# Optimization experiments

Measured on AMD Instinct MI355X. Metric: run time of the kernel, lower is better.

Reference implementation:

```python
import jax, jax.numpy as jnp
import numpy as np

D_MODEL = 768
D_INNER = 1536   # expand=2
D_STATE = 16
D_CONV = 4
DT_RANK = 48     # ceil(768/16)
B, T, N = 2, 4, 196


def _rmsnorm(x, w, eps=1e-5):
    var = jnp.mean(x * x, axis=-1, keepdims=True)
    return x * jax.lax.rsqrt(var + eps) * w


def _causal_dwconv(x, w, b):
    # x: (b, l, di), w: (di, k) depthwise, causal left-pad k-1
    xc = jnp.swapaxes(x, 1, 2)  # (b, di, l)
    out = jax.lax.conv_general_dilated(
        xc, w[:, None, :], window_strides=(1,), padding=[(D_CONV - 1, 0)],
        feature_group_count=D_INNER, dimension_numbers=('NCH', 'OIH', 'NCH'))
    return jnp.swapaxes(out + b[None, :, None], 1, 2)


def _selective_scan(u, dt, A, Bm, Cm, Dp):
    # u, dt: (b,l,di); Bm, Cm: (b,l,n); A: (di,n); Dp: (di,)
    dA = jnp.exp(dt[..., None] * A)                    # (b,l,di,n)
    dBu = (dt * u)[..., None] * Bm[:, :, None, :]      # (b,l,di,n)

    def step(h, inp):
        dA_t, dBu_t, C_t = inp
        h = dA_t * h + dBu_t                           # (b,di,n)
        return h, jnp.einsum('bdn,bn->bd', h, C_t)

    h0 = jnp.zeros((u.shape[0], D_INNER, D_STATE), u.dtype)
    _, ys = jax.lax.scan(step, h0, (jnp.swapaxes(dA, 0, 1),
                                    jnp.swapaxes(dBu, 0, 1),
                                    jnp.swapaxes(Cm, 0, 1)))
    return jnp.swapaxes(ys, 0, 1) + u * Dp


def _mamba(x, in_w, cw, cb, xp_w, dt_w, dt_b, A_log, Dp, out_w):
    xz = jnp.einsum('blc,ec->ble', x, in_w)            # (b,l,2*di)
    xb, z = jnp.split(xz, 2, axis=-1)
    xb = jax.nn.silu(_causal_dwconv(xb, cw, cb))
    x_dbl = jnp.einsum('bld,ed->ble', xb, xp_w)        # (b,l,dt_rank+2n)
    dt, Bm, Cm = jnp.split(x_dbl, [DT_RANK, DT_RANK + D_STATE], axis=-1)
    dt = jax.nn.softplus(jnp.einsum('blr,dr->bld', dt, dt_w) + dt_b)
    y = _selective_scan(xb, dt, -jnp.exp(A_log), Bm, Cm, Dp)
    y = y * jax.nn.silu(z)
    return jnp.einsum('bld,cd->blc', y, out_w)


def _block(x, i, norm_w, in_proj_w, conv_w, conv_b, x_proj_w, dt_proj_w,
           dt_proj_b, A_log, D, mix_out_w):
    # residual Mamba block: x + mixer(norm(x)); zero-initialized ssm/conv state
    return x + _mamba(_rmsnorm(x, norm_w[i]), in_proj_w[i], conv_w[i], conv_b[i],
                      x_proj_w[i], dt_proj_w[i], dt_proj_b[i], A_log[i], D[i],
                      mix_out_w[i])


def _bimamba(x, norm_w, in_proj_w, conv_w, conv_b, x_proj_w, dt_proj_w,
             dt_proj_b, A_log, D, mix_out_w, gate_w, gate_b, proj_w, proj_b):
    b, t, n, c = x.shape
    xs = x.reshape(b, t * n, c)
    params = (norm_w, in_proj_w, conv_w, conv_b, x_proj_w, dt_proj_w,
              dt_proj_b, A_log, D, mix_out_w)
    out_f = _block(xs, 0, *params)
    flip_t = lambda y: y.reshape(b, t, n, c)[:, ::-1].reshape(b, t * n, c)
    out_b = flip_t(_block(flip_t(xs), 1, *params))
    gate = jax.nn.sigmoid(
        jnp.einsum('blc,dc->bld', jnp.concatenate([out_f, out_b], -1), gate_w)
        + gate_b)
    out = gate * out_f + (1.0 - gate) * out_b
    out = jnp.einsum('bld,cd->blc', out, proj_w) + proj_b
    return out.reshape(b, t, n, c)


def setup_inputs() -> dict:
    key = jax.random.key(0)
    ks = jax.random.split(key, 12)
    s = 0.02
    a_log = jnp.broadcast_to(
        jnp.log(jnp.arange(1, D_STATE + 1, dtype=jnp.float32)),
        (2, D_INNER, D_STATE)).copy()
    return {
        'x': jax.random.normal(ks[0], (B, T, N, D_MODEL), jnp.float32),
        'norm_w': jnp.ones((2, D_MODEL), jnp.float32),
        'in_proj_w': jax.random.normal(ks[1], (2, 2 * D_INNER, D_MODEL), jnp.float32) * s,
        'conv_w': jax.random.normal(ks[2], (2, D_INNER, D_CONV), jnp.float32) * 0.2,
        'conv_b': jnp.zeros((2, D_INNER), jnp.float32),
        'x_proj_w': jax.random.normal(ks[3], (2, DT_RANK + 2 * D_STATE, D_INNER), jnp.float32) * s,
        'dt_proj_w': jax.random.normal(ks[4], (2, D_INNER, DT_RANK), jnp.float32) * s,
        'dt_proj_b': jax.random.normal(ks[5], (2, D_INNER), jnp.float32) * 0.5 - 4.0,
        'A_log': a_log,
        'D': jnp.ones((2, D_INNER), jnp.float32),
        'mix_out_w': jax.random.normal(ks[6], (2, D_MODEL, D_INNER), jnp.float32) * s,
        'gate_w': jax.random.normal(ks[7], (D_MODEL, 2 * D_MODEL), jnp.float32) * s,
        'gate_b': jnp.zeros((D_MODEL,), jnp.float32),
        'proj_w': jax.random.normal(ks[8], (D_MODEL, D_MODEL), jnp.float32) * s,
        'proj_b': jnp.zeros((D_MODEL,), jnp.float32),
    }


def reference(x, norm_w, in_proj_w, conv_w, conv_b, x_proj_w, dt_proj_w,
              dt_proj_b, A_log, D, mix_out_w, gate_w, gate_b, proj_w, proj_b):
    return _bimamba(x, norm_w, in_proj_w, conv_w, conv_b, x_proj_w, dt_proj_w,
                    dt_proj_b, A_log, D, mix_out_w, gate_w, gate_b, proj_w,
                    proj_b)
```

## Files before the change

### kernel.cpp

```cpp
#include <hip/hip_runtime.h>
#include <cstdint>
#include <cstddef>

#define BB 2
#define TT 4
#define NN 196
#define LL (TT*NN)
#define BLr (BB*LL)
#define CM 768
#define DI 1536
#define DS 16
#define DTR 48
#define XD 80
#define KSL (DI/4)
#define GCH 16
#define LC (LL/GCH)
#define NST (2*BB*DI*DS)

typedef short s16x8 __attribute__((ext_vector_type(8)));
typedef float f32x4 __attribute__((ext_vector_type(4)));

static __device__ __forceinline__ float sigmoidf_(float x) {
  return 1.f / (1.f + __expf(-x));
}
static __device__ __forceinline__ unsigned short f2bf(float f) {
  unsigned int u = __float_as_uint(f);
  unsigned int r = (u + 0x7fffu + ((u >> 16) & 1u)) >> 16;
  return (unsigned short)r;
}
static __device__ __forceinline__ float bf2f(unsigned short u) {
  return __uint_as_float(((unsigned int)u) << 16);
}
static __device__ __forceinline__ float softplusf_(float v) {
  return (v > 20.f) ? v : __logf(1.f + __expf(v));
}
static __device__ __forceinline__ void gload_lds16(const void* g, void* l) {
  __builtin_amdgcn_global_load_lds(
      (const __attribute__((address_space(1))) void*)g,
      (__attribute__((address_space(3))) void*)l, 16, 0, 0);
}

#define S_INW  4718592
#define S_OUTW 2359296
#define S_GATW 1179648
#define S_PRJW 589824
#define S_XPW  245760
#define S_DTW  196608
#define E0 S_INW
#define E1 (E0 + S_OUTW)
#define E2 (E1 + S_GATW)
#define E3 (E2 + S_PRJW)
#define E4 (E3 + S_XPW)
#define E5 (E4 + S_DTW)
#define NCAST ((E5)/256)

__global__ __launch_bounds__(256) void pre_k(const float* __restrict__ x,
    const float* __restrict__ nw, unsigned short* __restrict__ xn,
    const float* __restrict__ in_w, const float* __restrict__ out_w,
    const float* __restrict__ gate_w, const float* __restrict__ proj_w,
    const float* __restrict__ xp_w, const float* __restrict__ dt_w,
    unsigned short* __restrict__ dst)
{
  int blk = blockIdx.x;
  if (blk < 2*BLr) {
    int l   = blk % LL;
    int b   = (blk / LL) % BB;
    int dir = blk / (BB*LL);
    int lsrc = l;
    if (dir == 1) { int t = l / NN, n = l % NN; lsrc = (TT-1-t)*NN + n; }
    const float* xp = x + ((size_t)b*LL + lsrc)*CM;
    float s = 0.f;
    for (int c = threadIdx.x; c < CM; c += 256) { float v = xp[c]; s += v*v; }
    #pragma unroll
    for (int off = 32; off > 0; off >>= 1) s += __shfl_down(s, off);
    __shared__ float red[4];
    if ((threadIdx.x & 63) == 0) red[threadIdx.x >> 6] = s;
    __syncthreads();
    float tot = red[0] + red[1] + red[2] + red[3];
    float r = rsqrtf(tot * (1.f/CM) + 1e-5f);
    const float* w = nw + dir*CM;
    unsigned short* o = xn + (size_t)blk*CM;
    for (int c = threadIdx.x; c < CM; c += 256) o[c] = f2bf(xp[c] * r * w[c]);
  } else {
    int i = (blk - 2*BLr)*256 + threadIdx.x;
    float v;
    if (i < E0)       v = in_w[i];
    else if (i < E1)  v = out_w[i - E0];
    else if (i < E2)  v = gate_w[i - E1];
    else if (i < E3)  v = proj_w[i - E2];
    else if (i < E4)  v = xp_w[i - E3];
    else {
      int j = i - E4, r = j >> 6, c = j & 63;
      v = (c < 48) ? dt_w[r*48 + c] : 0.f;
    }
    dst[i] = f2bf(v);
  }
}

template <int BM, int BN>
__device__ __forceinline__ void gemm_core(
    const unsigned short* __restrict__ A, int lda,
    const unsigned short* __restrict__ W, int ldw,
    int M, int N, int K, int m0, int n0,
    short* As, short* Ws, f32x4 (*acc)[BN/32])
{
  const int tid = threadIdx.x;
  const int wv = tid >> 6, lane = tid & 63;
  const int wm0 = (wv >> 1)*(BM/2), wn0 = (wv & 1)*(BN/2);
  const int lm = lane & 15, g = lane >> 4;
  const int r8 = lane >> 3, ch = lane & 7;
  const int chs = ch ^ r8;
  constexpr int MT = BM/32, NT = BN/32;
  for (int k0 = 0; k0 < K; k0 += 64) {
    #pragma unroll
    for (int e = 0; e < BM/32; ++e) {
      int rb = e*32 + wv*8;
      int gr = m0 + rb + r8; if (gr >= M) gr = M - 1;
      gload_lds16(A + (size_t)gr*lda + k0 + chs*8, &As[rb*64 + lane*8]);
    }
    #pragma unroll
    for (int e = 0; e < BN/32; ++e) {
      int rb = e*32 + wv*8;
      int gn = n0 + rb + r8; if (gn >= N) gn = N - 1;
      gload_lds16(W + (size_t)gn*ldw + k0 + chs*8, &Ws[rb*64 + lane*8]);
    }
    __syncthreads();
    #pragma unroll
    for (int s = 0; s < 2; ++s) {
      s16x8 af[MT], bf[NT];
      #pragma unroll
      for (int i = 0; i < MT; ++i) {
        int R = wm0 + i*16 + lm;
        af[i] = *(const s16x8*)(&As[R*64 + (((s*4 + g) ^ (R & 7))*8)]);
      }
      #pragma unroll
      for (int j = 0; j < NT; ++j) {
        int Rn = wn0 + j*16 + lm;
        bf[j] = *(const s16x8*)(&Ws[Rn*64 + (((s*4 + g) ^ (Rn & 7))*8)]);
      }
      #pragma unroll
      for (int i = 0; i < MT; ++i)
        #pragma unroll
        for (int j = 0; j < NT; ++j)
          acc[i][j] = __builtin_amdgcn_mfma_f32_16x16x32_bf16(af[i], bf[j], acc[i][j], 0, 0, 0);
    }
    __syncthreads();
  }
}

__global__ __launch_bounds__(256, 2) void gemm_in_k(
    const unsigned short* __restrict__ xn, const unsigned short* __restrict__ w,
    unsigned short* __restrict__ xzout)
{
  __shared__ short As[128*64];
  __shared__ short Ws[128*64];
  const int dir = blockIdx.z;
  const unsigned short* A = xn + (size_t)dir*BLr*CM;
  const unsigned short* W = w  + (size_t)dir*2*DI*CM;
  unsigned short* C = xzout + (size_t)dir*BLr*2*DI;
  const int m0 = blockIdx.y*128, n0 = blockIdx.x*128;
  f32x4 acc[4][4];
  #pragma unroll
  for (int i = 0; i < 4; ++i)
    #pragma unroll
    for (int j = 0; j < 4; ++j) acc[i][j] = (f32x4){0.f,0.f,0.f,0.f};
  gemm_core<128,128>(A, CM, W, CM, BLr, 2*DI, CM, m0, n0, As, Ws, acc);
  const int tid = threadIdx.x, wv = tid >> 6, lane = tid & 63;
  const int wm0 = (wv >> 1)*64, wn0 = (wv & 1)*64;
  const int lm = lane & 15, g = lane >> 4;
  #pragma unroll
  for (int i = 0; i < 4; ++i) {
    int row = m0 + wm0 + i*16 + g*4;
    #pragma unroll
    for (int j = 0; j < 4; ++j) {
      int col = n0 + wn0 + j*16 + lm;
      #pragma unroll
      for (int r = 0; r < 4; ++r)
        if (row + r < BLr) C[(size_t)(row + r)*2*DI + col] = f2bf(acc[i][j][r]);
    }
  }
}

__global__ __launch_bounds__(256, 2) void convxproj_k(
    const unsigned short* __restrict__ xz, const float* __restrict__ cw,
    const float* __restrict__ cb, const unsigned short* __restrict__ xpw,
    unsigned short* __restrict__ ub, float* __restrict__ part)
{
  __shared__ short As[128*64];
  __shared__ short Ws[128*64];
  const int ks = blockIdx.x, mt = blockIdx.y, dir = blockIdx.z;
  const int m0 = mt*128;
  const int tid = threadIdx.x;
  const int wv = tid >> 6, lane = tid & 63;
  const int r8 = lane >> 3, ch = lane & 7;
  const int chs = ch ^ r8;
  const int lm = lane & 15, g = lane >> 4;
  const int wm0 = (wv >> 1)*64, wn0 = (wv & 1)*64;
  const unsigned short* XZ = xz + (size_t)dir*BLr*(2*DI);
  const unsigned short* W  = xpw + (size_t)dir*XD*DI + (size_t)ks*KSL;
  unsigned short* UB = ub + (size_t)dir*BLr*DI;
  f32x4 acc[4][4];
  #pragma unroll
  for (int i = 0; i < 4; ++i)
    #pragma unroll
    for (int j = 0; j < 4; ++j) acc[i][j] = (f32x4){0.f,0.f,0.f,0.f};

  for (int k0 = 0; k0 < KSL; k0 += 64) {
    const int di = ks*KSL + k0 + chs*8;
    #pragma unroll
    for (int e = 0; e < 4; ++e) {
      int rb = e*32 + wv*8;
      int gn = rb + r8; if (gn >= XD) gn = XD - 1;
      gload_lds16(W + (size_t)gn*DI + k0 + chs*8, &Ws[rb*64 + lane*8]);
    }
    f32x4 w4[8]; float cbv[8];
    #pragma unroll
    for (int j = 0; j < 8; ++j) {
      w4[j]  = *(const f32x4*)(cw + ((size_t)dir*DI + di + j)*4);
      cbv[j] = cb[dir*DI + di + j];
    }
    #pragma unroll
    for (int e = 0; e < 4; ++e) {
      int rb = e*32 + wv*8;
      int gr = m0 + rb + r8; if (gr >= BLr) gr = BLr - 1;
      int l = gr % LL;
      s16x8 tap[4];
      #pragma unroll
      for (int k = 0; k < 4; ++k) {
        int lp = l - 3 + k;
        if (lp >= 0) tap[k] = *(const s16x8*)(XZ + (size_t)(gr - 3 + k)*(2*DI) + di);
        else         tap[k] = (s16x8){0,0,0,0,0,0,0,0};
      }
      s16x8 outv;
      #pragma unroll
      for (int j = 0; j < 8; ++j) {
        float a = cbv[j];
        #pragma unroll
        for (int k = 0; k < 4; ++k)
          a = fmaf(w4[j][k], bf2f((unsigned short)tap[k][j]), a);
        float v = a * sigmoidf_(a);
        outv[j] = (short)f2bf(v);
      }
      *(s16x8*)(&As[rb*64 + lane*8]) = outv;
      *(s16x8*)(UB + (size_t)gr*DI + di) = outv;
    }
    __syncthreads();
    #pragma unroll
    for (int s = 0; s < 2; ++s) {
      s16x8 af[4], bfr[4];
      #pragma unroll
      for (int i = 0; i < 4; ++i) {
        int R = wm0 + i*16 + lm;
        af[i] = *(const s16x8*)(&As[R*64 + (((s*4 + g) ^ (R & 7))*8)]);
      }
      #pragma unroll
      for (int j = 0; j < 4; ++j) {
        int Rn = wn0 + j*16 + lm;
        bfr[j] = *(const s16x8*)(&Ws[Rn*64 + (((s*4 + g) ^ (Rn & 7))*8)]);
      }
      #pragma unroll
      for (int i = 0; i < 4; ++i)
        #pragma unroll
        for (int j = 0; j < 4; ++j)
          acc[i][j] = __builtin_amdgcn_mfma_f32_16x16x32_bf16(af[i], bfr[j], acc[i][j], 0, 0, 0);
    }
    __syncthreads();
  }
  float* P = part + ((size_t)(dir*4 + ks)*BLr)*XD;
  #pragma unroll
  for (int i = 0; i < 4; ++i) {
    int row = m0 + wm0 + i*16 + g*4;
    #pragma unroll
    for (int j = 0; j < 4; ++j) {
      int col = wn0 + j*16 + lm;
      if (col >= XD) continue;
      #pragma unroll
      for (int r = 0; r < 4; ++r)
        if (row + r < BLr) P[(size_t)(row + r)*XD + col] = acc[i][j][r];
    }
  }
}

__global__ __launch_bounds__(256, 4) void dtx_k(
    const float* __restrict__ part, const unsigned short* __restrict__ dtw,
    const float* __restrict__ dtb, float* __restrict__ dtv,
    float* __restrict__ xdbl)
{
  __shared__ short As[64*64];
  __shared__ short Ws[128*64];
  const int nt = blockIdx.x, mt = blockIdx.y, dir = blockIdx.z;
  const int m0 = mt*64, n0 = nt*128;
  const int tid = threadIdx.x;
  const int wv = tid >> 6, lane = tid & 63;
  const int r8 = lane >> 3, ch = lane & 7;
  const int chs = ch ^ r8;
  const int lm = lane & 15, g = lane >> 4;
  const int wm0 = (wv >> 1)*32, wn0 = (wv & 1)*64;
  const float* P0 = part + ((size_t)(dir*4))*BLr*XD;
  #pragma unroll
  for (int e = 0; e < 2; ++e) {
    int rb = e*32 + wv*8;
    int gr = m0 + rb + r8; if (gr >= BLr) gr = BLr - 1;
    s16x8 outv;
    if (chs < 6) {
      int c = chs*8;
      f32x4 s0 = {0.f,0.f,0.f,0.f}, s1 = {0.f,0.f,0.f,0.f};
      #pragma unroll
      for (int sl = 0; sl < 4; ++sl) {
        const float* p = P0 + ((size_t)sl*BLr + gr)*XD + c;
        s0 += *(const f32x4*)(p);
        s1 += *(const f32x4*)(p + 4);
      }
      #pragma unroll
      for (int j = 0; j < 4; ++j) { outv[j] = (short)f2bf(s0[j]); outv[4+j] = (short)f2bf(s1[j]); }
    } else {
      outv = (s16x8){0,0,0,0,0,0,0,0};
    }
    *(s16x8*)(&As[rb*64 + lane*8]) = outv;
  }
  #pragma unroll
  for (int e = 0; e < 4; ++e) {
    int rb = e*32 + wv*8;
    int gn = n0 + rb + r8;
    gload_lds16(dtw + (size_t)dir*DI*64 + (size_t)gn*64 + chs*8, &Ws[rb*64 + lane*8]);
  }
  __syncthreads();
  f32x4 acc[2][4];
  #pragma unroll
  for (int i = 0; i < 2; ++i)
    #pragma unroll
    for (int j = 0; j < 4; ++j) acc[i][j] = (f32x4){0.f,0.f,0.f,0.f};
  #pragma unroll
  for (int s = 0; s < 2; ++s) {
    s16x8 af[2], bfr[4];
    #pragma unroll
    for (int i = 0; i < 2; ++i) {
      int R = wm0 + i*16 + lm;
      af[i] = *(const s16x8*)(&As[R*64 + (((s*4 + g) ^ (R & 7))*8)]);
    }
    #pragma unroll
    for (int j = 0; j < 4; ++j) {
      int Rn = wn0 + j*16 + lm;
      bfr[j] = *(const s16x8*)(&Ws[Rn*64 + (((s*4 + g) ^ (Rn & 7))*8)]);
    }
    #pragma unroll
    for (int i = 0; i < 2; ++i)
      #pragma unroll
      for (int j = 0; j < 4; ++j)
        acc[i][j] = __builtin_amdgcn_mfma_f32_16x16x32_bf16(af[i], bfr[j], acc[i][j], 0, 0, 0);
  }
  float* C = dtv + (size_t)dir*BLr*DI;
  const float* bias = dtb + (size_t)dir*DI;
  #pragma unroll
  for (int i = 0; i < 2; ++i) {
    int row = m0 + wm0 + i*16 + g*4;
    #pragma unroll
    for (int j = 0; j < 4; ++j) {
      int col = n0 + wn0 + j*16 + lm;
      float bv = bias[col];
      #pragma unroll
      for (int r = 0; r < 4; ++r) {
        if (row + r >= BLr) continue;
        C[(size_t)(row + r)*DI + col] = softplusf_(acc[i][j][r] + bv);
      }
    }
  }
  if (nt == 0) {
    for (int idx = tid; idx < 64*XD; idx += 256) {
      int row = idx / XD, c = idx % XD;
      int gr = m0 + row;
      if (gr >= BLr) continue;
      float s = 0.f;
      #pragma unroll
      for (int sl = 0; sl < 4; ++sl)
        s += P0[((size_t)sl*BLr + gr)*XD + c];
      xdbl[((size_t)dir*BLr + gr)*XD + c] = s;
    }
  }
}

__global__ __launch_bounds__(256) void scanA_k(const float* __restrict__ dtv,
    const unsigned short* __restrict__ u, const float* __restrict__ xdbl,
    const float* __restrict__ A_log, float* __restrict__ carry,
    float* __restrict__ Pm)
{
  int bx = blockIdx.x;
  int g = bx & (GCH-1);
  int rest = bx / GCH;
  int dchunk = rest % (DI/64);
  int b   = (rest / (DI/64)) % BB;
  int dir = rest / ((DI/64)*BB);
  int tid = threadIdx.x;
  int dl = tid >> 2, q = tid & 3;
  int d = dchunk*64 + dl;
  size_t rb = ((size_t)dir*BB + b) * LL + (size_t)g*LC;
  const float* dtp = dtv + rb*DI + d;
  const unsigned short* up = u + rb*DI + d;
  const float* xB  = xdbl + rb*XD + DTR + 4*q;
  f32x4 al = *(const f32x4*)(A_log + ((size_t)dir*DI + d)*DS + 4*q);
  float Av[4];
  #pragma unroll
  for (int i = 0; i < 4; ++i) Av[i] = -__expf(al[i]);
  float h[4] = {0.f,0.f,0.f,0.f};
  float S = 0.f;
  float ndt[2], nu[2]; f32x4 nB[2];
  #pragma unroll
  for (int e = 0; e < 2; ++e) {
    ndt[e] = dtp[(size_t)e*DI];
    nu[e]  = bf2f(up[(size_t)e*DI]);
    nB[e]  = *(const f32x4*)(xB + (size_t)e*XD);
  }
  #pragma unroll 2
  for (int j = 0; j < LC; ++j) {
    int s = j & 1;
    float cdt = ndt[s], cu = nu[s];
    f32x4 cB = nB[s];
    int lp = j + 2;
    if (lp < LC) {
      ndt[s] = dtp[(size_t)lp*DI];
      nu[s]  = bf2f(up[(size_t)lp*DI]);
      nB[s]  = *(const f32x4*)(xB + (size_t)lp*XD);
    }
    float du = cdt * cu;
    S += cdt;
    #pragma unroll
    for (int i = 0; i < 4; ++i) {
      float dA = __expf(cdt * Av[i]);
      h[i] = fmaf(dA, h[i], du * cB[i]);
    }
  }
  size_t sid = (((size_t)(dir*BB + b)*DI + d)*DS + 4*q);
  f32x4 hc = {h[0], h[1], h[2], h[3]};
  f32x4 pc = {__expf(Av[0]*S), __expf(Av[1]*S), __expf(Av[2]*S), __expf(Av[3]*S)};
  *(f32x4*)(carry + (size_t)g*NST + sid) = hc;
  *(f32x4*)(Pm    + (size_t)g*NST + sid) = pc;
}

__global__ __launch_bounds__(256) void scanB_k(float* __restrict__ carry,
    const float* __restrict__ Pm)
{
  int sid = blockIdx.x*256 + threadIdx.x;
  float h = 0.f;
  #pragma unroll
  for (int g = 0; g < GCH; ++g) {
    float c = carry[(size_t)g*NST + sid];
    float p = Pm[(size_t)g*NST + sid];
    carry[(size_t)g*NST + sid] = h;
    h = fmaf(p, h, c);
  }
}

__global__ __launch_bounds__(256) void scanC_k(const float* __restrict__ dtv,
    const unsigned short* __restrict__ u, const unsigned short* __restrict__ xz,
    const float* __restrict__ xdbl, const float* __restrict__ A_log,
    const float* __restrict__ Dp, const float* __restrict__ h_in,
    unsigned short* __restrict__ y)
{
  int bx = blockIdx.x;
  int g = bx & (GCH-1);
  int rest = bx / GCH;
  int dchunk = rest % (DI/64);
  int b   = (rest / (DI/64)) % BB;
  int dir = rest / ((DI/64)*BB);
  int tid = threadIdx.x;
  int dl = tid >> 2, q = tid & 3;
  int d = dchunk*64 + dl;
  size_t rb = ((size_t)dir*BB + b) * LL + (size_t)g*LC;
  const float* dtp = dtv + rb*DI + d;
  const unsigned short* up = u + rb*DI + d;
  const unsigned short* zp = xz + rb*(2*DI) + DI + d;
  const float* xB  = xdbl + rb*XD + DTR + 4*q;
  const float* xC  = xB + DS;
  unsigned short* yp = y + rb*DI + d;
  f32x4 al = *(const f32x4*)(A_log + ((size_t)dir*DI + d)*DS + 4*q);
  float Av[4];
  #pragma unroll
  for (int i = 0; i < 4; ++i) Av[i] = -__expf(al[i]);
  float Dd = Dp[dir*DI + d];
  size_t sid = (((size_t)(dir*BB + b)*DI + d)*DS + 4*q);
  f32x4 h4 = *(const f32x4*)(h_in + (size_t)g*NST + sid);
  float h[4] = {h4[0], h4[1], h4[2], h4[3]};
  float ndt[2], nu[2], nz[2]; f32x4 nB[2], nC[2];
  #pragma unroll
  for (int e = 0; e < 2; ++e) {
    ndt[e] = dtp[(size_t)e*DI];
    nu[e]  = bf2f(up[(size_t)e*DI]);
    nz[e]  = bf2f(zp[(size_t)e*(2*DI)]);
    nB[e]  = *(const f32x4*)(xB + (size_t)e*XD);
    nC[e]  = *(const f32x4*)(xC + (size_t)e*XD);
  }
  #pragma unroll 2
  for (int j = 0; j < LC; ++j) {
    int s = j & 1;
    float cdt = ndt[s], cu = nu[s], cz = nz[s];
    f32x4 cB = nB[s], cC = nC[s];
    int lp = j + 2;
    if (lp < LC) {
      ndt[s] = dtp[(size_t)lp*DI];
      nu[s]  = bf2f(up[(size_t)lp*DI]);
      nz[s]  = bf2f(zp[(size_t)lp*(2*DI)]);
      nB[s]  = *(const f32x4*)(xB + (size_t)lp*XD);
      nC[s]  = *(const f32x4*)(xC + (size_t)lp*XD);
    }
    float du = cdt * cu;
    float acc = 0.f;
    #pragma unroll
    for (int i = 0; i < 4; ++i) {
      float dA = __expf(cdt * Av[i]);
      h[i] = fmaf(dA, h[i], du * cB[i]);
      acc = fmaf(h[i], cC[i], acc);
    }
    acc += __shfl_xor(acc, 1);
    acc += __shfl_xor(acc, 2);
    if (q == 0) {
      float yv = (acc + cu * Dd) * (cz * sigmoidf_(cz));
      yp[(size_t)j*DI] = f2bf(yv);
    }
  }
}

__global__ __launch_bounds__(256, 4) void gemm_outp_k(
    const unsigned short* __restrict__ yb, const unsigned short* __restrict__ w,
    const float* __restrict__ x, unsigned short* __restrict__ cat)
{
  __shared__ short As[64*64];
  __shared__ short Ws[128*64];
  const int dir = blockIdx.z;
  const unsigned short* A = yb + (size_t)dir*BLr*DI;
  const unsigned short* W = w + (size_t)dir*CM*DI;
  const int m0 = blockIdx.y*64, n0 = blockIdx.x*128;
  f32x4 acc[2][4];
  #pragma unroll
  for (int i = 0; i < 2; ++i)
    #pragma unroll
    for (int j = 0; j < 4; ++j) acc[i][j] = (f32x4){0.f,0.f,0.f,0.f};
  gemm_core<64,128>(A, DI, W, DI, BLr, CM, DI, m0, n0, As, Ws, acc);
  const int tid = threadIdx.x, wv = tid >> 6, lane = tid & 63;
  const int wm0 = (wv >> 1)*32, wn0 = (wv & 1)*64;
  const int lm = lane & 15, g = lane >> 4;
  #pragma unroll
  for (int i = 0; i < 2; ++i) {
    int row = m0 + wm0 + i*16 + g*4;
    #pragma unroll
    for (int j = 0; j < 4; ++j) {
      int col = n0 + wn0 + j*16 + lm;
      #pragma unroll
      for (int r = 0; r < 4; ++r) {
        int rr = row + r;
        if (rr >= BLr) continue;
        int rt = rr;
        if (dir == 1) {
          int l = rr % LL, b = rr / LL;
          int t = l / NN, nn = l % NN;
          rt = b*LL + (TT-1-t)*NN + nn;
        }
        float v = x[(size_t)rt*CM + col] + acc[i][j][r];
        cat[(size_t)rt*(2*CM) + dir*CM + col] = f2bf(v);
      }
    }
  }
}

__global__ __launch_bounds__(256, 4) void gemm_gate_k(
    const unsigned short* __restrict__ cat, const unsigned short* __restrict__ w,
    const float* __restrict__ gb, unsigned short* __restrict__ mixb)
{
  __shared__ short As[64*64];
  __shared__ short Ws[64*64];
  const int m0 = blockIdx.y*64, n0 = blockIdx.x*64;
  f32x4 acc[2][2];
  #pragma unroll
  for (int i = 0; i < 2; ++i)
    #pragma unroll
    for (int j = 0; j < 2; ++j) acc[i][j] = (f32x4){0.f,0.f,0.f,0.f};
  gemm_core<64,64>(cat, 2*CM, w, 2*CM, BLr, CM, 2*CM, m0, n0, As, Ws, acc);
  const int tid = threadIdx.x, wv = tid >> 6, lane = tid & 63;
  const int wm0 = (wv >> 1)*32, wn0 = (wv & 1)*32;
  const int lm = lane & 15, g = lane >> 4;
  #pragma unroll
  for (int i = 0; i < 2; ++i) {
    int row = m0 + wm0 + i*16 + g*4;
    #pragma unroll
    for (int j = 0; j < 2; ++j) {
      int col = n0 + wn0 + j*16 + lm;
      float bv = gb[col];
      #pragma unroll
      for (int r = 0; r < 4; ++r) {
        int rr = row + r;
        if (rr >= BLr) continue;
        float gg = sigmoidf_(acc[i][j][r] + bv);
        float fv = bf2f(cat[(size_t)rr*(2*CM) + col]);
        float bo = bf2f(cat[(size_t)rr*(2*CM) + CM + col]);
        mixb[(size_t)rr*CM + col] = f2bf(gg*fv + (1.f - gg)*bo);
      }
    }
  }
}

__global__ __launch_bounds__(256, 4) void gemm_proj_k(
    const unsigned short* __restrict__ mixb, const unsigned short* __restrict__ w,
    const float* __restrict__ pb, float* __restrict__ out)
{
  __shared__ short As[64*64];
  __shared__ short Ws[64*64];
  const int m0 = blockIdx.y*64, n0 = blockIdx.x*64;
  f32x4 acc[2][2];
  #pragma unroll
  for (int i = 0; i < 2; ++i)
    #pragma unroll
    for (int j = 0; j < 2; ++j) acc[i][j] = (f32x4){0.f,0.f,0.f,0.f};
  gemm_core<64,64>(mixb, CM, w, CM, BLr, CM, CM, m0, n0, As, Ws, acc);
  const int tid = threadIdx.x, wv = tid >> 6, lane = tid & 63;
  const int wm0 = (wv >> 1)*32, wn0 = (wv & 1)*32;
  const int lm = lane & 15, g = lane >> 4;
  #pragma unroll
  for (int i = 0; i < 2; ++i) {
    int row = m0 + wm0 + i*16 + g*4;
    #pragma unroll
    for (int j = 0; j < 2; ++j) {
      int col = n0 + wn0 + j*16 + lm;
      float bv = pb[col];
      #pragma unroll
      for (int r = 0; r < 4; ++r)
        if (row + r < BLr) out[(size_t)(row + r)*CM + col] = acc[i][j][r] + bv;
    }
  }
}

extern "C" void kernel_launch(void* const* d_in, const int* in_sizes, int n_in,
                              void* d_out, int out_size, void* d_ws, size_t ws_size,
                              hipStream_t stream)
{
  (void)in_sizes; (void)n_in; (void)out_size; (void)ws_size;
  const float* x      = (const float*)d_in[0];
  const float* norm_w = (const float*)d_in[1];
  const float* in_w   = (const float*)d_in[2];
  const float* conv_w = (const float*)d_in[3];
  const float* conv_b = (const float*)d_in[4];
  const float* xp_w   = (const float*)d_in[5];
  const float* dt_w   = (const float*)d_in[6];
  const float* dt_b   = (const float*)d_in[7];
  const float* A_log  = (const float*)d_in[8];
  const float* Dp     = (const float*)d_in[9];
  const float* out_w  = (const float*)d_in[10];
  const float* gate_w = (const float*)d_in[11];
  const float* gate_b = (const float*)d_in[12];
  const float* proj_w = (const float*)d_in[13];
  const float* proj_b = (const float*)d_in[14];
  float* out = (float*)d_out;
  char* wsb  = (char*)d_ws;

  unsigned short* w_all   = (unsigned short*)(wsb + 0);
  unsigned short* in_w_b  = w_all;
  unsigned short* out_w_b = w_all + E0;
  unsigned short* gate_w_b= w_all + E1;
  unsigned short* proj_w_b= w_all + E2;
  unsigned short* xp_w_b  = w_all + E3;
  unsigned short* dt_w_b  = w_all + E4;
  unsigned short* xz_b = (unsigned short*)(wsb + 18579456);
  unsigned short* ub   = (unsigned short*)(wsb + 37847040);
  float* xdbl  = (float*)(wsb + 57114624);
  float* dtvb  = (float*)(wsb + 58118144);
  unsigned short* y_b = (unsigned short*)(wsb + 77385728);
  unsigned short* tmp = (unsigned short*)(wsb + 87019520);
  unsigned short* cat_b = (unsigned short*)(wsb + 106287104);
  unsigned short* mix_b = (unsigned short*)(wsb + 111104000);

  unsigned short* xn_b = tmp;
  float* part = (float*)(wsb + 0);
  float* carry = (float*)(wsb + 0);
  float* Pmat  = (float*)(wsb + 87019520 + 524288);

  pre_k<<<2*BLr + NCAST, 256, 0, stream>>>(
      x, norm_w, xn_b, in_w, out_w, gate_w, proj_w, xp_w, dt_w, w_all);
  gemm_in_k<<<dim3(3072/128, (BLr+127)/128, 2), 256, 0, stream>>>(
      xn_b, in_w_b, xz_b);
  convxproj_k<<<dim3(4, (BLr+127)/128, 2), 256, 0, stream>>>(
      xz_b, conv_w, conv_b, xp_w_b, ub, part);
  dtx_k<<<dim3(DI/128, (BLr+63)/64, 2), 256, 0, stream>>>(
      part, dt_w_b, dt_b, dtvb, xdbl);
  scanA_k<<<2*BB*(DI/64)*GCH, 256, 0, stream>>>(
      dtvb, ub, xdbl, A_log, carry, Pmat);
  scanB_k<<<NST/256, 256, 0, stream>>>(carry, Pmat);
  scanC_k<<<2*BB*(DI/64)*GCH, 256, 0, stream>>>(
      dtvb, ub, xz_b, xdbl, A_log, Dp, carry, y_b);
  gemm_outp_k<<<dim3(CM/128, (BLr+63)/64, 2), 256, 0, stream>>>(
      y_b, out_w_b, x, cat_b);
  gemm_gate_k<<<dim3(CM/64, (BLr+63)/64, 1), 256, 0, stream>>>(
      cat_b, gate_w_b, gate_b, mix_b);
  gemm_proj_k<<<dim3(CM/64, (BLr+63)/64, 1), 256, 0, stream>>>(
      mix_b, proj_w_b, proj_b, out);
}
```

Before: 317.7 us.

## Fuse all stages into one persistent megakernel with software grid barriers

```diff
diff --git a/kernel.cpp b/kernel.cpp
--- a/kernel.cpp
+++ b/kernel.cpp
@@ -12,10 +12,10 @@
 #define DS 16
 #define DTR 48
 #define XD 80
-#define KSL (DI/4)
 #define GCH 16
 #define LC (LL/GCH)
 #define NST (2*BB*DI*DS)
+#define NB 512
 
 typedef short s16x8 __attribute__((ext_vector_type(8)));
 typedef float f32x4 __attribute__((ext_vector_type(4)));
@@ -52,53 +52,40 @@
 #define E3 (E2 + S_PRJW)
 #define E4 (E3 + S_XPW)
 #define E5 (E4 + S_DTW)
-#define NCAST ((E5)/256)
-
-__global__ __launch_bounds__(256) void pre_k(const float* __restrict__ x,
-    const float* __restrict__ nw, unsigned short* __restrict__ xn,
-    const float* __restrict__ in_w, const float* __restrict__ out_w,
-    const float* __restrict__ gate_w, const float* __restrict__ proj_w,
-    const float* __restrict__ xp_w, const float* __restrict__ dt_w,
-    unsigned short* __restrict__ dst)
-{
-  int blk = blockIdx.x;
-  if (blk < 2*BLr) {
-    int l   = blk % LL;
-    int b   = (blk / LL) % BB;
-    int dir = blk / (BB*LL);
-    int lsrc = l;
-    if (dir == 1) { int t = l / NN, n = l % NN; lsrc = (TT-1-t)*NN + n; }
-    const float* xp = x + ((size_t)b*LL + lsrc)*CM;
-    float s = 0.f;
-    for (int c = threadIdx.x; c < CM; c += 256) { float v = xp[c]; s += v*v; }
-    #pragma unroll
-    for (int off = 32; off > 0; off >>= 1) s += __shfl_down(s, off);
-    __shared__ float red[4];
-    if ((threadIdx.x & 63) == 0) red[threadIdx.x >> 6] = s;
-    __syncthreads();
-    float tot = red[0] + red[1] + red[2] + red[3];
-    float r = rsqrtf(tot * (1.f/CM) + 1e-5f);
-    const float* w = nw + dir*CM;
-    unsigned short* o = xn + (size_t)blk*CM;
-    for (int c = threadIdx.x; c < CM; c += 256) o[c] = f2bf(xp[c] * r * w[c]);
-  } else {
-    int i = (blk - 2*BLr)*256 + threadIdx.x;
-    float v;
-    if (i < E0)       v = in_w[i];
-    else if (i < E1)  v = out_w[i - E0];
-    else if (i < E2)  v = gate_w[i - E1];
-    else if (i < E3)  v = proj_w[i - E2];
-    else if (i < E4)  v = xp_w[i - E3];
-    else {
-      int j = i - E4, r = j >> 6, c = j & 63;
-      v = (c < 48) ? dt_w[r*48 + c] : 0.f;
-    }
-    dst[i] = f2bf(v);
-  }
+
+#define O_WALL  0u
+#define O_XZ    18579456u
+#define O_UB    37847040u
+#define O_XDBLB 47480832u
+#define O_XDBL  48000000u
+#define O_DTV   50000000u
+#define O_Y     70000000u
+#define O_CARRY 80000000u
+#define O_PM    87000000u
+#define O_XN    94000000u
+#define O_PART  99000000u
+#define O_CAT   112000000u
+#define O_MIX   117000000u
+#define O_OPART 120000000u
+#define O_GPART 149000000u
+#define O_PPART 178000000u
+#define O_BAR   198000000u
+
+static __device__ __forceinline__ void gridbar(int* bar, int slot) {
+  __syncthreads();
+  if (threadIdx.x == 0) {
+    __threadfence();
+    atomicAdd(&bar[slot], 1);
+    while (__hip_atomic_load(&bar[slot], __ATOMIC_RELAXED,
+                             __HIP_MEMORY_SCOPE_AGENT) < NB)
+      __builtin_amdgcn_s_sleep(1);
+    __threadfence();
+  }
+  __syncthreads();
 }
 
 template <int BM, int BN>
-__device__ __forceinline__ void gemm_core(
+static __device__ __forceinline__ void gemm_core(
     const unsigned short* __restrict__ A, int lda,
     const unsigned short* __restrict__ W, int ldw,
     int M, int N, int K, int m0, int n0,
@@ -148,23 +135,9 @@
   }
 }
 
-__global__ __launch_bounds__(256, 2) void gemm_in_k(
-    const unsigned short* __restrict__ xn, const unsigned short* __restrict__ w,
-    unsigned short* __restrict__ xzout)
+static __device__ __forceinline__ void epi_part(
+    f32x4 (*acc)[4], float* P, int ldp, int m0, int n0)
 {
-  __shared__ short As[128*64];
-  __shared__ short Ws[128*64];
-  const int dir = blockIdx.z;
-  const unsigned short* A = xn + (size_t)dir*BLr*CM;
-  const unsigned short* W = w  + (size_t)dir*2*DI*CM;
-  unsigned short* C = xzout + (size_t)dir*BLr*2*DI;
-  const int m0 = blockIdx.y*128, n0 = blockIdx.x*128;
-  f32x4 acc[4][4];
-  #pragma unroll
-  for (int i = 0; i < 4; ++i)
-    #pragma unroll
-    for (int j = 0; j < 4; ++j) acc[i][j] = (f32x4){0.f,0.f,0.f,0.f};
-  gemm_core<128,128>(A, CM, W, CM, BLr, 2*DI, CM, m0, n0, As, Ws, acc);
   const int tid = threadIdx.x, wv = tid >> 6, lane = tid & 63;
   const int wm0 = (wv >> 1)*64, wn0 = (wv & 1)*64;
   const int lm = lane & 15, g = lane >> 4;
@@ -176,454 +149,469 @@
       int col = n0 + wn0 + j*16 + lm;
       #pragma unroll
       for (int r = 0; r < 4; ++r)
-        if (row + r < BLr) C[(size_t)(row + r)*2*DI + col] = f2bf(acc[i][j][r]);
-    }
-  }
-}
-
-__global__ __launch_bounds__(256, 2) void convxproj_k(
-    const unsigned short* __restrict__ xz, const float* __restrict__ cw,
-    const float* __restrict__ cb, const unsigned short* __restrict__ xpw,
-    unsigned short* __restrict__ ub, float* __restrict__ part)
+        if (row + r < BLr) P[(size_t)(row + r)*ldp + col] = acc[i][j][r];
+    }
+  }
+}
+static __device__ __forceinline__ void epi_bf16(
+    f32x4 (*acc)[4], unsigned short* C, int ldc, int m0, int n0)
 {
+  const int tid = threadIdx.x, wv = tid >> 6, lane = tid & 63;
+  const int wm0 = (wv >> 1)*64, wn0 = (wv & 1)*64;
+  const int lm = lane & 15, g = lane >> 4;
+  #pragma unroll
+  for (int i = 0; i < 4; ++i) {
+    int row = m0 + wm0 + i*16 + g*4;
+    #pragma unroll
+    for (int j = 0; j < 4; ++j) {
+      int col = n0 + wn0 + j*16 + lm;
+      #pragma unroll
+      for (int r = 0; r < 4; ++r)
+        if (row + r < BLr) C[(size_t)(row + r)*ldc + col] = f2bf(acc[i][j][r]);
+    }
+  }
+}
+
+__global__ __launch_bounds__(256, 2) void mega_k(
+    const float* __restrict__ x, const float* __restrict__ norm_w,
+    const float* __restrict__ in_w, const float* __restrict__ conv_w,
+    const float* __restrict__ conv_b, const float* __restrict__ xp_w,
+    const float* __restrict__ dt_w, const float* __restrict__ dt_b,
+    const float* __restrict__ A_log, const float* __restrict__ Dp,
+    const float* __restrict__ out_w, const float* __restrict__ gate_w,
+    const float* __restrict__ gate_b, const float* __restrict__ proj_w,
+    const float* __restrict__ proj_b, float* __restrict__ out,
+    char* __restrict__ wsb)
+{
+  unsigned short* w_all  = (unsigned short*)(wsb + O_WALL);
+  unsigned short* out_w_b  = w_all + E0;
+  unsigned short* gate_w_b = w_all + E1;
+  unsigned short* proj_w_b = w_all + E2;
+  unsigned short* xp_w_b   = w_all + E3;
+  unsigned short* dt_w_b   = w_all + E4;
+  unsigned short* xz_b   = (unsigned short*)(wsb + O_XZ);
+  unsigned short* ub     = (unsigned short*)(wsb + O_UB);
+  unsigned short* xdbl_b = (unsigned short*)(wsb + O_XDBLB);
+  float* xdbl   = (float*)(wsb + O_XDBL);
+  float* dtvb   = (float*)(wsb + O_DTV);
+  unsigned short* y_b    = (unsigned short*)(wsb + O_Y);
+  float* carry  = (float*)(wsb + O_CARRY);
+  float* Pmat   = (float*)(wsb + O_PM);
+  unsigned short* xn_b   = (unsigned short*)(wsb + O_XN);
+  float* part   = (float*)(wsb + O_PART);
+  unsigned short* cat_b  = (unsigned short*)(wsb + O_CAT);
+  unsigned short* mix_b  = (unsigned short*)(wsb + O_MIX);
+  float* opart  = (float*)(wsb + O_OPART);
+  float* gpart  = (float*)(wsb + O_GPART);
+  float* ppart  = (float*)(wsb + O_PPART);
+  int* bar      = (int*)(wsb + O_BAR);
+
   __shared__ short As[128*64];
   __shared__ short Ws[128*64];
-  const int ks = blockIdx.x, mt = blockIdx.y, dir = blockIdx.z;
-  const int m0 = mt*128;
-  const int tid = threadIdx.x;
+  __shared__ float red[4];
+
+  const int bid = blockIdx.x, tid = threadIdx.x;
   const int wv = tid >> 6, lane = tid & 63;
   const int r8 = lane >> 3, ch = lane & 7;
   const int chs = ch ^ r8;
-  const int lm = lane & 15, g = lane >> 4;
-  const int wm0 = (wv >> 1)*64, wn0 = (wv & 1)*64;
-  const unsigned short* XZ = xz + (size_t)dir*BLr*(2*DI);
-  const unsigned short* W  = xpw + (size_t)dir*XD*DI + (size_t)ks*KSL;
-  unsigned short* UB = ub + (size_t)dir*BLr*DI;
-  f32x4 acc[4][4];
-  #pragma unroll
-  for (int i = 0; i < 4; ++i)
-    #pragma unroll
-    for (int j = 0; j < 4; ++j) acc[i][j] = (f32x4){0.f,0.f,0.f,0.f};
-
-  for (int k0 = 0; k0 < KSL; k0 += 64) {
-    const int di = ks*KSL + k0 + chs*8;
-    #pragma unroll
-    for (int e = 0; e < 4; ++e) {
-      int rb = e*32 + wv*8;
-      int gn = rb + r8; if (gn >= XD) gn = XD - 1;
-      gload_lds16(W + (size_t)gn*DI + k0 + chs*8, &Ws[rb*64 + lane*8]);
-    }
-    f32x4 w4[8]; float cbv[8];
-    #pragma unroll
-    for (int j = 0; j < 8; ++j) {
-      w4[j]  = *(const f32x4*)(cw + ((size_t)dir*DI + di + j)*4);
-      cbv[j] = cb[dir*DI + di + j];
-    }
-    #pragma unroll
-    for (int e = 0; e < 4; ++e) {
-      int rb = e*32 + wv*8;
-      int gr = m0 + rb + r8; if (gr >= BLr) gr = BLr - 1;
-      int l = gr % LL;
-      s16x8 tap[4];
-      #pragma unroll
-      for (int k = 0; k < 4; ++k) {
-        int lp = l - 3 + k;
-        if (lp >= 0) tap[k] = *(const s16x8*)(XZ + (size_t)(gr - 3 + k)*(2*DI) + di);
-        else         tap[k] = (s16x8){0,0,0,0,0,0,0,0};
-      }
-      s16x8 outv;
+  const int lm = lane & 15, g4 = lane >> 4;
+
+  for (int row = bid; row < 2*BLr; row += NB) {
+    int l   = row % LL;
+    int b   = (row / LL) % BB;
+    int dir = row / (BB*LL);
+    int lsrc = l;
+    if (dir == 1) { int t = l / NN, n = l % NN; lsrc = (TT-1-t)*NN + n; }
+    const float* xp = x + ((size_t)b*LL + lsrc)*CM;
+    float s = 0.f;
+    for (int c = tid; c < CM; c += 256) { float v = xp[c]; s += v*v; }
+    #pragma unroll
+    for (int off = 32; off > 0; off >>= 1) s += __shfl_down(s, off);
+    if ((tid & 63) == 0) red[tid >> 6] = s;
+    __syncthreads();
+    float tot = red[0] + red[1] + red[2] + red[3];
+    float rs = rsqrtf(tot * (1.f/CM) + 1e-5f);
+    const float* w = norm_w + dir*CM;
+    unsigned short* o = xn_b + (size_t)row*CM;
+    for (int c = tid; c < CM; c += 256) o[c] = f2bf(xp[c] * rs * w[c]);
+    __syncthreads();
+  }
+  for (int i = bid*256 + tid; i < E5; i += NB*256) {
+    float v;
+    if (i < E0)       v = in_w[i];
+    else if (i < E1)  v = out_w[i - E0];
+    else if (i < E2)  v = gate_w[i - E1];
+    else if (i < E3)  v = proj_w[i - E2];
+    else if (i < E4)  v = xp_w[i - E3];
+    else {
+      int j = i - E4, r = j >> 6, c = j & 63;
+      v = (c < 48) ? dt_w[r*48 + c] : 0.f;
+    }
+    w_all[i] = f2bf(v);
+  }
+  gridbar(bar, 0);
+
+  for (int t = bid; t < 624; t += NB) {
+    int nt = t % 24, mt = (t/24) % 13, dir = t/312;
+    const unsigned short* A = xn_b + (size_t)dir*BLr*CM;
+    const unsigned short* W = w_all + (size_t)dir*2*DI*CM;
+    unsigned short* C = xz_b + (size_t)dir*BLr*2*DI;
+    f32x4 acc[4][4];
+    #pragma unroll
+    for (int i = 0; i < 4; ++i)
+      #pragma unroll
+      for (int j = 0; j < 4; ++j) acc[i][j] = (f32x4){0.f,0.f,0.f,0.f};
+    gemm_core<128,128>(A, CM, W, CM, BLr, 2*DI, CM, mt*128, nt*128, As, Ws, acc);
+    epi_bf16(acc, C, 2*DI, mt*128, nt*128);
+  }
+  gridbar(bar, 1);
+
+  for (int t = bid; t < 312; t += NB) {
+    int ks = t % 12, mt = (t/12) % 13, dir = t/156;
+    const int m0 = mt*128;
+    const int wm0 = (wv >> 1)*64, wn0 = (wv & 1)*64;
+    const unsigned short* XZ = xz_b + (size_t)dir*BLr*(2*DI);
+    const unsigned short* W  = xp_w_b + (size_t)dir*XD*DI + ks*128;
+    unsigned short* UB = ub + (size_t)dir*BLr*DI;
+    f32x4 acc[4][4];
+    #pragma unroll
+    for (int i = 0; i < 4; ++i)
+      #pragma unroll
+      for (int j = 0; j < 4; ++j) acc[i][j] = (f32x4){0.f,0.f,0.f,0.f};
+    for (int k0 = 0; k0 < 128; k0 += 64) {
+      const int di = ks*128 + k0 + chs*8;
+      #pragma unroll
+      for (int e = 0; e < 4; ++e) {
+        int rb = e*32 + wv*8;
+        int gn = rb + r8; if (gn >= XD) gn = XD - 1;
+        gload_lds16(W + (size_t)gn*DI + k0 + chs*8, &Ws[rb*64 + lane*8]);
+      }
+      f32x4 w4[8]; float cbv[8];
       #pragma unroll
       for (int j = 0; j < 8; ++j) {
-        float a = cbv[j];
-        #pragma unroll
-        for (int k = 0; k < 4; ++k)
-          a = fmaf(w4[j][k], bf2f((unsigned short)tap[k][j]), a);
-        float v = a * sigmoidf_(a);
-        outv[j] = (short)f2bf(v);
-      }
-      *(s16x8*)(&As[rb*64 + lane*8]) = outv;
-      *(s16x8*)(UB + (size_t)gr*DI + di) = outv;
-    }
-    __syncthreads();
-    #pragma unroll
-    for (int s = 0; s < 2; ++s) {
-      s16x8 af[4], bfr[4];
+        w4[j]  = *(const f32x4*)(conv_w + ((size_t)dir*DI + di + j)*4);
+        cbv[j] = conv_b[dir*DI + di + j];
+      }
+      #pragma unroll
+      for (int e = 0; e < 4; ++e) {
+        int rb = e*32 + wv*8;
+        int gr = m0 + rb + r8; if (gr >= BLr) gr = BLr - 1;
+        int l = gr % LL;
+        s16x8 tap[4];
+        #pragma unroll
+        for (int k = 0; k < 4; ++k) {
+          int lp = l - 3 + k;
+          if (lp >= 0) tap[k] = *(const s16x8*)(XZ + (size_t)(gr - 3 + k)*(2*DI) + di);
+          else         tap[k] = (s16x8){0,0,0,0,0,0,0,0};
+        }
+        s16x8 outv;
+        #pragma unroll
+        for (int j = 0; j < 8; ++j) {
+          float a = cbv[j];
+          #pragma unroll
+          for (int k = 0; k < 4; ++k)
+            a = fmaf(w4[j][k], bf2f((unsigned short)tap[k][j]), a);
+          float v = a * sigmoidf_(a);
+          outv[j] = (short)f2bf(v);
+        }
+        *(s16x8*)(&As[rb*64 + lane*8]) = outv;
+        *(s16x8*)(UB + (size_t)gr*DI + di) = outv;
+      }
+      __syncthreads();
+      #pragma unroll
+      for (int s = 0; s < 2; ++s) {
+        s16x8 af[4], bfr[4];
+        #pragma unroll
+        for (int i = 0; i < 4; ++i) {
+          int R = wm0 + i*16 + lm;
+          af[i] = *(const s16x8*)(&As[R*64 + (((s*4 + g4) ^ (R & 7))*8)]);
+        }
+        #pragma unroll
+        for (int j = 0; j < 4; ++j) {
+          int Rn = wn0 + j*16 + lm;
+          bfr[j] = *(const s16x8*)(&Ws[Rn*64 + (((s*4 + g4) ^ (Rn & 7))*8)]);
+        }
+        #pragma unroll
+        for (int i = 0; i < 4; ++i)
+          #pragma unroll
+          for (int j = 0; j < 4; ++j)
+            acc[i][j] = __builtin_amdgcn_mfma_f32_16x16x32_bf16(af[i], bfr[j], acc[i][j], 0, 0, 0);
+      }
+      __syncthreads();
+    }
+    float* P = part + ((size_t)(dir*12 + ks)*BLr)*XD;
+    #pragma unroll
+    for (int i = 0; i < 4; ++i) {
+      int row = m0 + wm0 + i*16 + g4*4;
+      #pragma unroll
+      for (int j = 0; j < 4; ++j) {
+        int col = wn0 + j*16 + lm;
+        if (col >= XD) continue;
+        #pragma unroll
+        for (int r = 0; r < 4; ++r)
+          if (row + r < BLr) P[(size_t)(row + r)*XD + col] = acc[i][j][r];
+      }
+    }
+  }
+  gridbar(bar, 2);
+
+  for (int i = bid*256 + tid; i < 2*BLr*XD; i += NB*256) {
+    int c = i % XD;
+    int r = i / XD;
+    int dir = r / BLr, row = r % BLr;
+    float s = 0.f;
+    #pragma unroll
+    for (int sl = 0; sl < 12; ++sl)
+      s += part[((size_t)(dir*12 + sl)*BLr + row)*XD + c];
+    xdbl[i] = s;
+    if (c < DTR) xdbl_b[(size_t)r*64 + c] = f2bf(s);
+  }
+  for (int i = bid*256 + tid; i < 2*BLr*16; i += NB*256) {
+    int r = i / 16, c = 48 + (i & 15);
+    xdbl_b[(size_t)r*64 + c] = 0;
+  }
+  gridbar(bar, 3);
+
+  for (int t = bid; t < 312; t += NB) {
+    int nt = t % 12, mt = (t/12) % 13, dir = t/156;
+    const unsigned short* A = xdbl_b + (size_t)dir*BLr*64;
+    const unsigned short* W = dt_w_b + (size_t)dir*DI*64;
+    f32x4 acc[4][4];
+    #pragma unroll
+    for (int i = 0; i < 4; ++i)
+      #pragma unroll
+      for (int j = 0; j < 4; ++j) acc[i][j] = (f32x4){0.f,0.f,0.f,0.f};
+    gemm_core<128,128>(A, 64, W, 64, BLr, DI, 64, mt*128, nt*128, As, Ws, acc);
+    float* C = dtvb + (size_t)dir*BLr*DI;
+    const float* bias = dt_b + (size_t)dir*DI;
+    const int wm0 = (wv >> 1)*64, wn0 = (wv & 1)*64;
+    #pragma unroll
+    for (int i = 0; i < 4; ++i) {
+      int row = mt*128 + wm0 + i*16 + g4*4;
+      #pragma unroll
+      for (int j = 0; j < 4; ++j) {
+        int col = nt*128 + wn0 + j*16 + lm;
+        float bv = bias[col];
+        #pragma unroll
+        for (int r = 0; r < 4; ++r)
+          if (row + r < BLr)
+            C[(size_t)(row + r)*DI + col] = softplusf_(acc[i][j][r] + bv);
+      }
+    }
+  }
+  gridbar(bar, 4);
+
+  for (int v = bid; v < 2*BB*(DI/64)*GCH; v += NB) {
+    int g = v & (GCH-1);
+    int rest = v / GCH;
+    int dchunk = rest % (DI/64);
+    int b   = (rest / (DI/64)) % BB;
+    int dir = rest / ((DI/64)*BB);
+    int dl = tid >> 2, q = tid & 3;
+    int d = dchunk*64 + dl;
+    size_t rb = ((size_t)dir*BB + b) * LL + (size_t)g*LC;
+    const float* dtp = dtvb + rb*DI + d;
+    const unsigned short* up = ub + rb*DI + d;
+    const float* xB  = xdbl + rb*XD + DTR + 4*q;
+    f32x4 al = *(const f32x4*)(A_log + ((size_t)dir*DI + d)*DS + 4*q);
+    float Av[4];
+    #pragma unroll
+    for (int i = 0; i < 4; ++i) Av[i] = -__expf(al[i]);
+    float h[4] = {0.f,0.f,0.f,0.f};
+    float S = 0.f;
+    float ndt[2], nu[2]; f32x4 nB[2];
+    #pragma unroll
+    for (int e = 0; e < 2; ++e) {
+      ndt[e] = dtp[(size_t)e*DI];
+      nu[e]  = bf2f(up[(size_t)e*DI]);
+      nB[e]  = *(const f32x4*)(xB + (size_t)e*XD);
+    }
+    #pragma unroll 2
+    for (int j = 0; j < LC; ++j) {
+      int s = j & 1;
+      float cdt = ndt[s], cu = nu[s];
+      f32x4 cB = nB[s];
+      int lp = j + 2;
+      if (lp < LC) {
+        ndt[s] = dtp[(size_t)lp*DI];
+        nu[s]  = bf2f(up[(size_t)lp*DI]);
+        nB[s]  = *(const f32x4*)(xB + (size_t)lp*XD);
+      }
+      float du = cdt * cu;
+      S += cdt;
       #pragma unroll
       for (int i = 0; i < 4; ++i) {
-        int R = wm0 + i*16 + lm;
-        af[i] = *(const s16x8*)(&As[R*64 + (((s*4 + g) ^ (R & 7))*8)]);
-      }
-      #pragma unroll
-      for (int j = 0; j < 4; ++j) {
-        int Rn = wn0 + j*16 + lm;
-        bfr[j] = *(const s16x8*)(&Ws[Rn*64 + (((s*4 + g) ^ (Rn & 7))*8)]);
-      }
-      #pragma unroll
-      for (int i = 0; i < 4; ++i)
-        #pragma unroll
-        for (int j = 0; j < 4; ++j)
-          acc[i][j] = __builtin_amdgcn_mfma_f32_16x16x32_bf16(af[i], bfr[j], acc[i][j], 0, 0, 0);
-    }
-    __syncthreads();
-  }
-  float* P = part + ((size_t)(dir*4 + ks)*BLr)*XD;
-  #pragma unroll
-  for (int i = 0; i < 4; ++i) {
-    int row = m0 + wm0 + i*16 + g*4;
-    #pragma unroll
-    for (int j = 0; j < 4; ++j) {
-      int col = wn0 + j*16 + lm;
-      if (col >= XD) continue;
-      #pragma unroll
-      for (int r = 0; r < 4; ++r)
-        if (row + r < BLr) P[(size_t)(row + r)*XD + col] = acc[i][j][r];
-    }
-  }
-}
-
-__global__ __launch_bounds__(256, 4) void dtx_k(
-    const float* __restrict__ part, const unsigned short* __restrict__ dtw,
-    const float* __restrict__ dtb, float* __restrict__ dtv,
-    float* __restrict__ xdbl)
-{
-  __shared__ short As[64*64];
-  __shared__ short Ws[128*64];
-  const int nt = blockIdx.x, mt = blockIdx.y, dir = blockIdx.z;
-  const int m0 = mt*64, n0 = nt*128;
-  const int tid = threadIdx.x;
-  const int wv = tid >> 6, lane = tid & 63;
-  const int r8 = lane >> 3, ch = lane & 7;
-  const int chs = ch ^ r8;
-  const int lm = lane & 15, g = lane >> 4;
-  const int wm0 = (wv >> 1)*32, wn0 = (wv & 1)*64;
-  const float* P0 = part + ((size_t)(dir*4))*BLr*XD;
-  #pragma unroll
-  for (int e = 0; e < 2; ++e) {
-    int rb = e*32 + wv*8;
-    int gr = m0 + rb + r8; if (gr >= BLr) gr = BLr - 1;
-    s16x8 outv;
-    if (chs < 6) {
-      int c = chs*8;
-      f32x4 s0 = {0.f,0.f,0.f,0.f}, s1 = {0.f,0.f,0.f,0.f};
-      #pragma unroll
-      for (int sl = 0; sl < 4; ++sl) {
-        const float* p = P0 + ((size_t)sl*BLr + gr)*XD + c;
-        s0 += *(const f32x4*)(p);
-        s1 += *(const f32x4*)(p + 4);
-      }
-      #pragma unroll
-      for (int j = 0; j < 4; ++j) { outv[j] = (short)f2bf(s0[j]); outv[4+j] = (short)f2bf(s1[j]); }
-    } else {
-      outv = (s16x8){0,0,0,0,0,0,0,0};
-    }
-    *(s16x8*)(&As[rb*64 + lane*8]) = outv;
-  }
-  #pragma unroll
-  for (int e = 0; e < 4; ++e) {
-    int rb = e*32 + wv*8;
-    int gn = n0 + rb + r8;
-    gload_lds16(dtw + (size_t)dir*DI*64 + (size_t)gn*64 + chs*8, &Ws[rb*64 + lane*8]);
-  }
-  __syncthreads();
-  f32x4 acc[2][4];
-  #pragma unroll
-  for (int i = 0; i < 2; ++i)
-    #pragma unroll
-    for (int j = 0; j < 4; ++j) acc[i][j] = (f32x4){0.f,0.f,0.f,0.f};
-  #pragma unroll
-  for (int s = 0; s < 2; ++s) {
-    s16x8 af[2], bfr[4];
-    #pragma unroll
-    for (int i = 0; i < 2; ++i) {
-      int R = wm0 + i*16 + lm;
-      af[i] = *(const s16x8*)(&As[R*64 + (((s*4 + g) ^ (R & 7))*8)]);
-    }
-    #pragma unroll
-    for (int j = 0; j < 4; ++j) {
-      int Rn = wn0 + j*16 + lm;
-      bfr[j] = *(const s16x8*)(&Ws[Rn*64 + (((s*4 + g) ^ (Rn & 7))*8)]);
-    }
-    #pragma unroll
-    for (int i = 0; i < 2; ++i)
-      #pragma unroll
-      for (int j = 0; j < 4; ++j)
-        acc[i][j] = __builtin_amdgcn_mfma_f32_16x16x32_bf16(af[i], bfr[j], acc[i][j], 0, 0, 0);
-  }
-  float* C = dtv + (size_t)dir*BLr*DI;
-  const float* bias = dtb + (size_t)dir*DI;
-  #pragma unroll
-  for (int i = 0; i < 2; ++i) {
-    int row = m0 + wm0 + i*16 + g*4;
-    #pragma unroll
-    for (int j = 0; j < 4; ++j) {
-      int col = n0 + wn0 + j*16 + lm;
-      float bv = bias[col];
-      #pragma unroll
-      for (int r = 0; r < 4; ++r) {
-        if (row + r >= BLr) continue;
-        C[(size_t)(row + r)*DI + col] = softplusf_(acc[i][j][r] + bv);
-      }
-    }
-  }
-  if (nt == 0) {
-    for (int idx = tid; idx < 64*XD; idx += 256) {
-      int row = idx / XD, c = idx % XD;
-      int gr = m0 + row;
-      if (gr >= BLr) continue;
-      float s = 0.f;
-      #pragma unroll
-      for (int sl = 0; sl < 4; ++sl)
-        s += P0[((size_t)sl*BLr + gr)*XD + c];
-      xdbl[((size_t)dir*BLr + gr)*XD + c] = s;
-    }
-  }
-}
-
-__global__ __launch_bounds__(256) void scanA_k(const float* __restrict__ dtv,
-    const unsigned short* __restrict__ u, const float* __restrict__ xdbl,
-    const float* __restrict__ A_log, float* __restrict__ carry,
-    float* __restrict__ Pm)
-{
-  int bx = blockIdx.x;
-  int g = bx & (GCH-1);
-  int rest = bx / GCH;
-  int dchunk = rest % (DI/64);
-  int b   = (rest / (DI/64)) % BB;
-  int dir = rest / ((DI/64)*BB);
-  int tid = threadIdx.x;
-  int dl = tid >> 2, q = tid & 3;
-  int d = dchunk*64 + dl;
-  size_t rb = ((size_t)dir*BB + b) * LL + (size_t)g*LC;
-  const float* dtp = dtv + rb*DI + d;
-  const unsigned short* up = u + rb*DI + d;
-  const float* xB  = xdbl + rb*XD + DTR + 4*q;
-  f32x4 al = *(const f32x4*)(A_log + ((size_t)dir*DI + d)*DS + 4*q);
-  float Av[4];
-  #pragma unroll
-  for (int i = 0; i < 4; ++i) Av[i] = -__expf(al[i]);
-  float h[4] = {0.f,0.f,0.f,0.f};
-  float S = 0.f;
-  float ndt[2], nu[2]; f32x4 nB[2];
-  #pragma unroll
-  for (int e = 0; e < 2; ++e) {
-    ndt[e] = dtp[(size_t)e*DI];
-    nu[e]  = bf2f(up[(size_t)e*DI]);
-    nB[e]  = *(const f32x4*)(xB + (size_t)e*XD);
-  }
-  #pragma unroll 2
-  for (int j = 0; j < LC; ++j) {
-    int s = j & 1;
-    float cdt = ndt[s], cu = nu[s];
-    f32x4 cB = nB[s];
-    int lp = j + 2;
-    if (lp < LC) {
-      ndt[s] = dtp[(size_t)lp*DI];
-      nu[s]  = bf2f(up[(size_t)lp*DI]);
-      nB[s]  = *(const f32x4*)(xB + (size_t)lp*XD);
-    }
-    float du = cdt * cu;
-    S += cdt;
-    #pragma unroll
-    for (int i = 0; i < 4; ++i) {
-      float dA = __expf(cdt * Av[i]);
-      h[i] = fmaf(dA, h[i], du * cB[i]);
-    }
-  }
-  size_t sid = (((size_t)(dir*BB + b)*DI + d)*DS + 4*q);
-  f32x4 hc = {h[0], h[1], h[2], h[3]};
-  f32x4 pc = {__expf(Av[0]*S), __expf(Av[1]*S), __expf(Av[2]*S), __expf(Av[3]*S)};
-  *(f32x4*)(carry + (size_t)g*NST + sid) = hc;
-  *(f32x4*)(Pm    + (size_t)g*NST + sid) = pc;
-}
-
-__global__ __launch_bounds__(256) void scanB_k(float* __restrict__ carry,
-    const float* __restrict__ Pm)
-{
-  int sid = blockIdx.x*256 + threadIdx.x;
-  float h = 0.f;
-  #pragma unroll
-  for (int g = 0; g < GCH; ++g) {
-    float c = carry[(size_t)g*NST + sid];
-    float p = Pm[(size_t)g*NST + sid];
-    carry[(size_t)g*NST + sid] = h;
-    h = fmaf(p, h, c);
-  }
-}
-
-__global__ __launch_bounds__(256) void scanC_k(const float* __restrict__ dtv,
-    const unsigned short* __restrict__ u, const unsigned short* __restrict__ xz,
-    const float* __restrict__ xdbl, const float* __restrict__ A_log,
-    const float* __restrict__ Dp, const float* __restrict__ h_in,
-    unsigned short* __restrict__ y)
-{
-  int bx = blockIdx.x;
-  int g = bx & (GCH-1);
-  int rest = bx / GCH;
-  int dchunk = rest % (DI/64);
-  int b   = (rest / (DI/64)) % BB;
-  int dir = rest / ((DI/64)*BB);
-  int tid = threadIdx.x;
-  int dl = tid >> 2, q = tid & 3;
-  int d = dchunk*64 + dl;
-  size_t rb = ((size_t)dir*BB + b) * LL + (size_t)g*LC;
-  const float* dtp = dtv + rb*DI + d;
-  const unsigned short* up = u + rb*DI + d;
-  const unsigned short* zp = xz + rb*(2*DI) + DI + d;
-  const float* xB  = xdbl + rb*XD + DTR + 4*q;
-  const float* xC  = xB + DS;
-  unsigned short* yp = y + rb*DI + d;
-  f32x4 al = *(const f32x4*)(A_log + ((size_t)dir*DI + d)*DS + 4*q);
-  float Av[4];
-  #pragma unroll
-  for (int i = 0; i < 4; ++i) Av[i] = -__expf(al[i]);
-  float Dd = Dp[dir*DI + d];
-  size_t sid = (((size_t)(dir*BB + b)*DI + d)*DS + 4*q);
-  f32x4 h4 = *(const f32x4*)(h_in + (size_t)g*NST + sid);
-  float h[4] = {h4[0], h4[1], h4[2], h4[3]};
-  float ndt[2], nu[2], nz[2]; f32x4 nB[2], nC[2];
-  #pragma unroll
-  for (int e = 0; e < 2; ++e) {
-    ndt[e] = dtp[(size_t)e*DI];
-    nu[e]  = bf2f(up[(size_t)e*DI]);
-    nz[e]  = bf2f(zp[(size_t)e*(2*DI)]);
-    nB[e]  = *(const f32x4*)(xB + (size_t)e*XD);
-    nC[e]  = *(const f32x4*)(xC + (size_t)e*XD);
-  }
-  #pragma unroll 2
-  for (int j = 0; j < LC; ++j) {
-    int s = j & 1;
-    float cdt = ndt[s], cu = nu[s], cz = nz[s];
-    f32x4 cB = nB[s], cC = nC[s];
-    int lp = j + 2;
-    if (lp < LC) {
-      ndt[s] = dtp[(size_t)lp*DI];
-      nu[s]  = bf2f(up[(size_t)lp*DI]);
-      nz[s]  = bf2f(zp[(size_t)lp*(2*DI)]);
-      nB[s]  = *(const f32x4*)(xB + (size_t)lp*XD);
-      nC[s]  = *(const f32x4*)(xC + (size_t)lp*XD);
-    }
-    float du = cdt * cu;
-    float acc = 0.f;
-    #pragma unroll
-    for (int i = 0; i < 4; ++i) {
-      float dA = __expf(cdt * Av[i]);
-      h[i] = fmaf(dA, h[i], du * cB[i]);
-      acc = fmaf(h[i], cC[i], acc);
-    }
-    acc += __shfl_xor(acc, 1);
-    acc += __shfl_xor(acc, 2);
-    if (q == 0) {
-      float yv = (acc + cu * Dd) * (cz * sigmoidf_(cz));
-      yp[(size_t)j*DI] = f2bf(yv);
-    }
-  }
-}
-
-__global__ __launch_bounds__(256, 4) void gemm_outp_k(
-    const unsigned short* __restrict__ yb, const unsigned short* __restrict__ w,
-    const float* __restrict__ x, unsigned short* __restrict__ cat)
-{
-  __shared__ short As[64*64];
-  __shared__ short Ws[128*64];
-  const int dir = blockIdx.z;
-  const unsigned short* A = yb + (size_t)dir*BLr*DI;
-  const unsigned short* W = w + (size_t)dir*CM*DI;
-  const int m0 = blockIdx.y*64, n0 = blockIdx.x*128;
-  f32x4 acc[2][4];
-  #pragma unroll
-  for (int i = 0; i < 2; ++i)
-    #pragma unroll
-    for (int j = 0; j < 4; ++j) acc[i][j] = (f32x4){0.f,0.f,0.f,0.f};
-  gemm_core<64,128>(A, DI, W, DI, BLr, CM, DI, m0, n0, As, Ws, acc);
-  const int tid = threadIdx.x, wv = tid >> 6, lane = tid & 63;
-  const int wm0 = (wv >> 1)*32, wn0 = (wv & 1)*64;
-  const int lm = lane & 15, g = lane >> 4;
-  #pragma unroll
-  for (int i = 0; i < 2; ++i) {
-    int row = m0 + wm0 + i*16 + g*4;
-    #pragma unroll
-    for (int j = 0; j < 4; ++j) {
-      int col = n0 + wn0 + j*16 + lm;
-      #pragma unroll
-      for (int r = 0; r < 4; ++r) {
-        int rr = row + r;
-        if (rr >= BLr) continue;
-        int rt = rr;
-        if (dir == 1) {
-          int l = rr % LL, b = rr / LL;
-          int t = l / NN, nn = l % NN;
-          rt = b*LL + (TT-1-t)*NN + nn;
-        }
-        float v = x[(size_t)rt*CM + col] + acc[i][j][r];
-        cat[(size_t)rt*(2*CM) + dir*CM + col] = f2bf(v);
-      }
-    }
-  }
-}
-
-__global__ __launch_bounds__(256, 4) void gemm_gate_k(
-    const unsigned short* __restrict__ cat, const unsigned short* __restrict__ w,
-    const float* __restrict__ gb, unsigned short* __restrict__ mixb)
-{
-  __shared__ short As[64*64];
-  __shared__ short Ws[64*64];
-  const int m0 = blockIdx.y*64, n0 = blockIdx.x*64;
-  f32x4 acc[2][2];
-  #pragma unroll
-  for (int i = 0; i < 2; ++i)
-    #pragma unroll
-    for (int j = 0; j < 2; ++j) acc[i][j] = (f32x4){0.f,0.f,0.f,0.f};
-  gemm_core<64,64>(cat, 2*CM, w, 2*CM, BLr, CM, 2*CM, m0, n0, As, Ws, acc);
-  const int tid = threadIdx.x, wv = tid >> 6, lane = tid & 63;
-  const int wm0 = (wv >> 1)*32, wn0 = (wv & 1)*32;
-  const int lm = lane & 15, g = lane >> 4;
-  #pragma unroll
-  for (int i = 0; i < 2; ++i) {
-    int row = m0 + wm0 + i*16 + g*4;
-    #pragma unroll
-    for (int j = 0; j < 2; ++j) {
-      int col = n0 + wn0 + j*16 + lm;
-      float bv = gb[col];
-      #pragma unroll
-      for (int r = 0; r < 4; ++r) {
-        int rr = row + r;
-        if (rr >= BLr) continue;
-        float gg = sigmoidf_(acc[i][j][r] + bv);
-        float fv = bf2f(cat[(size_t)rr*(2*CM) + col]);
-        float bo = bf2f(cat[(size_t)rr*(2*CM) + CM + col]);
-        mixb[(size_t)rr*CM + col] = f2bf(gg*fv + (1.f - gg)*bo);
-      }
-    }
-  }
-}
-
-__global__ __launch_bounds__(256, 4) void gemm_proj_k(
-    const unsigned short* __restrict__ mixb, const unsigned short* __restrict__ w,
-    const float* __restrict__ pb, float* __restrict__ out)
-{
-  __shared__ short As[64*64];
-  __shared__ short Ws[64*64];
-  const int m0 = blockIdx.y*64, n0 = blockIdx.x*64;
-  f32x4 acc[2][2];
-  #pragma unroll
-  for (int i = 0; i < 2; ++i)
-    #pragma unroll
-    for (int j = 0; j < 2; ++j) acc[i][j] = (f32x4){0.f,0.f,0.f,0.f};
-  gemm_core<64,64>(mixb, CM, w, CM, BLr, CM, CM, m0, n0, As, Ws, acc);
-  const int tid = threadIdx.x, wv = tid >> 6, lane = tid & 63;
-  const int wm0 = (wv >> 1)*32, wn0 = (wv & 1)*32;
-  const int lm = lane & 15, g = lane >> 4;
-  #pragma unroll
-  for (int i = 0; i < 2; ++i) {
-    int row = m0 + wm0 + i*16 + g*4;
-    #pragma unroll
-    for (int j = 0; j < 2; ++j) {
-      int col = n0 + wn0 + j*16 + lm;
-      float bv = pb[col];
-      #pragma unroll
-      for (int r = 0; r < 4; ++r)
-        if (row + r < BLr) out[(size_t)(row + r)*CM + col] = acc[i][j][r] + bv;
-    }
+        float dA = __expf(cdt * Av[i]);
+        h[i] = fmaf(dA, h[i], du * cB[i]);
+      }
+    }
+    size_t sid = (((size_t)(dir*BB + b)*DI + d)*DS + 4*q);
+    f32x4 hc = {h[0], h[1], h[2], h[3]};
+    f32x4 pc = {__expf(Av[0]*S), __expf(Av[1]*S), __expf(Av[2]*S), __expf(Av[3]*S)};
+    *(f32x4*)(carry + (size_t)g*NST + sid) = hc;
+    *(f32x4*)(Pmat  + (size_t)g*NST + sid) = pc;
+  }
+  gridbar(bar, 5);
+
+  for (int v = bid; v < NST/256; v += NB) {
+    int sid = v*256 + tid;
+    float h = 0.f;
+    #pragma unroll
+    for (int g = 0; g < GCH; ++g) {
+      float c = carry[(size_t)g*NST + sid];
+      float p = Pmat[(size_t)g*NST + sid];
+      carry[(size_t)g*NST + sid] = h;
+      h = fmaf(p, h, c);
+    }
+  }
+  gridbar(bar, 6);
+
+  for (int v = bid; v < 2*BB*(DI/64)*GCH; v += NB) {
+    int g = v & (GCH-1);
+    int rest = v / GCH;
+    int dchunk = rest % (DI/64);
+    int b   = (rest / (DI/64)) % BB;
+    int dir = rest / ((DI/64)*BB);
+    int dl = tid >> 2, q = tid & 3;
+    int d = dchunk*64 + dl;
+    size_t rb = ((size_t)dir*BB + b) * LL + (size_t)g*LC;
+    const float* dtp = dtvb + rb*DI + d;
+    const unsigned short* up = ub + rb*DI + d;
+    const unsigned short* zp = xz_b + rb*(2*DI) + DI + d;
+    const float* xB  = xdbl + rb*XD + DTR + 4*q;
+    const float* xC  = xB + DS;
+    unsigned short* yp = y_b + rb*DI + d;
+    f32x4 al = *(const f32x4*)(A_log + ((size_t)dir*DI + d)*DS + 4*q);
+    float Av[4];
+    #pragma unroll
+    for (int i = 0; i < 4; ++i) Av[i] = -__expf(al[i]);
+    float Dd = Dp[dir*DI + d];
+    size_t sid = (((size_t)(dir*BB + b)*DI + d)*DS + 4*q);
+    f32x4 h4 = *(const f32x4*)(carry + (size_t)g*NST + sid);
+    float h[4] = {h4[0], h4[1], h4[2], h4[3]};
+    float ndt[2], nu[2], nz[2]; f32x4 nB[2], nC[2];
+    #pragma unroll
+    for (int e = 0; e < 2; ++e) {
+      ndt[e] = dtp[(size_t)e*DI];
+      nu[e]  = bf2f(up[(size_t)e*DI]);
+      nz[e]  = bf2f(zp[(size_t)e*(2*DI)]);
+      nB[e]  = *(const f32x4*)(xB + (size_t)e*XD);
+      nC[e]  = *(const f32x4*)(xC + (size_t)e*XD);
+    }
+    #pragma unroll 2
+    for (int j = 0; j < LC; ++j) {
+      int s = j & 1;
+      float cdt = ndt[s], cu = nu[s], cz = nz[s];
+      f32x4 cB = nB[s], cC = nC[s];
+      int lp = j + 2;
+      if (lp < LC) {
+        ndt[s] = dtp[(size_t)lp*DI];
+        nu[s]  = bf2f(up[(size_t)lp*DI]);
+        nz[s]  = bf2f(zp[(size_t)lp*(2*DI)]);
+        nB[s]  = *(const f32x4*)(xB + (size_t)lp*XD);
+        nC[s]  = *(const f32x4*)(xC + (size_t)lp*XD);
+      }
+      float du = cdt * cu;
+      float acc = 0.f;
+      #pragma unroll
+      for (int i = 0; i < 4; ++i) {
+        float dA = __expf(cdt * Av[i]);
+        h[i] = fmaf(dA, h[i], du * cB[i]);
+        acc = fmaf(h[i], cC[i], acc);
+      }
+      acc += __shfl_xor(acc, 1);
+      acc += __shfl_xor(acc, 2);
+      if (q == 0) {
+        float yv = (acc + cu * Dd) * (cz * sigmoidf_(cz));
+        yp[(size_t)j*DI] = f2bf(yv);
+      }
+    }
+  }
+  gridbar(bar, 7);
+
+  for (int t = bid; t < 468; t += NB) {
+    int nt = t % 6, mt = (t/6) % 13, ks = (t/78) % 3, dir = t/234;
+    const unsigned short* A = y_b + (size_t)dir*BLr*DI + ks*512;
+    const unsigned short* W = out_w_b + (size_t)dir*CM*DI + ks*512;
+    f32x4 acc[4][4];
+    #pragma unroll
+    for (int i = 0; i < 4; ++i)
+      #pragma unroll
+      for (int j = 0; j < 4; ++j) acc[i][j] = (f32x4){0.f,0.f,0.f,0.f};
+    gemm_core<128,128>(A, DI, W, DI, BLr, CM, 512, mt*128, nt*128, As, Ws, acc);
+    float* P = opart + ((size_t)(dir*3 + ks)*BLr)*CM;
+    epi_part(acc, P, CM, mt*128, nt*128);
+  }
+  gridbar(bar, 8);
+
+  for (int i = bid*256 + tid; i < 2*BLr*CM; i += NB*256) {
+    int col = i % CM;
+    int ra  = i / CM;
+    int dir = ra / BLr, rr = ra % BLr;
+    float s = opart[((size_t)(dir*3 + 0)*BLr + rr)*CM + col]
+            + opart[((size_t)(dir*3 + 1)*BLr + rr)*CM + col]
+            + opart[((size_t)(dir*3 + 2)*BLr + rr)*CM + col];
+    int rt = rr;
+    if (dir == 1) {
+      int l = rr % LL, b = rr / LL;
+      int t = l / NN, nn = l % NN;
+      rt = b*LL + (TT-1-t)*NN + nn;
+    }
+    float v = x[(size_t)rt*CM + col] + s;
+    cat_b[(size_t)rt*(2*CM) + dir*CM + col] = f2bf(v);
+  }
+  gridbar(bar, 9);
+
+  for (int t = bid; t < 468; t += NB) {
+    int nt = t % 6, mt = (t/6) % 13, ks = t/78;
+    const unsigned short* A = cat_b + ks*256;
+    const unsigned short* W = gate_w_b + ks*256;
+    f32x4 acc[4][4];
+    #pragma unroll
+    for (int i = 0; i < 4; ++i)
+      #pragma unroll
+      for (int j = 0; j < 4; ++j) acc[i][j] = (f32x4){0.f,0.f,0.f,0.f};
+    gemm_core<128,128>(A, 2*CM, W, 2*CM, BLr, CM, 256, mt*128, nt*128, As, Ws, acc);
+    float* P = gpart + (size_t)ks*BLr*CM;
+    epi_part(acc, P, CM, mt*128, nt*128);
+  }
+  gridbar(bar, 10);
+
+  for (int i = bid*256 + tid; i < BLr*CM; i += NB*256) {
+    int col = i % CM, rr = i / CM;
+    float s = gate_b[col];
+    #pragma unroll
+    for (int ks = 0; ks < 6; ++ks)
+      s += gpart[((size_t)ks*BLr + rr)*CM + col];
+    float gg = sigmoidf_(s);
+    float fv = bf2f(cat_b[(size_t)rr*(2*CM) + col]);
+    float bo = bf2f(cat_b[(size_t)rr*(2*CM) + CM + col]);
+    mix_b[i] = f2bf(gg*fv + (1.f - gg)*bo);
+  }
+  gridbar(bar, 11);
+
+  for (int t = bid; t < 312; t += NB) {
+    int nt = t % 6, mt = (t/6) % 13, ks = t/78;
+    const unsigned short* A = mix_b + ks*192;
+    const unsigned short* W = proj_w_b + ks*192;
+    f32x4 acc[4][4];
+    #pragma unroll
+    for (int i = 0; i < 4; ++i)
+      #pragma unroll
+      for (int j = 0; j < 4; ++j) acc[i][j] = (f32x4){0.f,0.f,0.f,0.f};
+    gemm_core<128,128>(A, CM, W, CM, BLr, CM, 192, mt*128, nt*128, As, Ws, acc);
+    float* P = ppart + (size_t)ks*BLr*CM;
+    epi_part(acc, P, CM, mt*128, nt*128);
+  }
+  gridbar(bar, 12);
+
+  for (int i = bid*256 + tid; i < BLr*CM; i += NB*256) {
+    int col = i % CM, rr = i / CM;
+    float s = proj_b[col];
+    #pragma unroll
+    for (int ks = 0; ks < 4; ++ks)
+      s += ppart[((size_t)ks*BLr + rr)*CM + col];
+    out[i] = s;
   }
 }
 
@@ -650,44 +638,8 @@
   float* out = (float*)d_out;
   char* wsb  = (char*)d_ws;
 
-  unsigned short* w_all   = (unsigned short*)(wsb + 0);
-  unsigned short* in_w_b  = w_all;
-  unsigned short* out_w_b = w_all + E0;
-  unsigned short* gate_w_b= w_all + E1;
-  unsigned short* proj_w_b= w_all + E2;
-  unsigned short* xp_w_b  = w_all + E3;
-  unsigned short* dt_w_b  = w_all + E4;
-  unsigned short* xz_b = (unsigned short*)(wsb + 18579456);
-  unsigned short* ub   = (unsigned short*)(wsb + 37847040);
-  float* xdbl  = (float*)(wsb + 57114624);
-  float* dtvb  = (float*)(wsb + 58118144);
-  unsigned short* y_b = (unsigned short*)(wsb + 77385728);
-  unsigned short* tmp = (unsigned short*)(wsb + 87019520);
-  unsigned short* cat_b = (unsigned short*)(wsb + 106287104);
-  unsigned short* mix_b = (unsigned short*)(wsb + 111104000);
-
-  unsigned short* xn_b = tmp;
-  float* part = (float*)(wsb + 0);
-  float* carry = (float*)(wsb + 0);
-  float* Pmat  = (float*)(wsb + 87019520 + 524288);
-
-  pre_k<<<2*BLr + NCAST, 256, 0, stream>>>(
-      x, norm_w, xn_b, in_w, out_w, gate_w, proj_w, xp_w, dt_w, w_all);
-  gemm_in_k<<<dim3(3072/128, (BLr+127)/128, 2), 256, 0, stream>>>(
-      xn_b, in_w_b, xz_b);
-  convxproj_k<<<dim3(4, (BLr+127)/128, 2), 256, 0, stream>>>(
-      xz_b, conv_w, conv_b, xp_w_b, ub, part);
-  dtx_k<<<dim3(DI/128, (BLr+63)/64, 2), 256, 0, stream>>>(
-      part, dt_w_b, dt_b, dtvb, xdbl);
-  scanA_k<<<2*BB*(DI/64)*GCH, 256, 0, stream>>>(
-      dtvb, ub, xdbl, A_log, carry, Pmat);
-  scanB_k<<<NST/256, 256, 0, stream>>>(carry, Pmat);
-  scanC_k<<<2*BB*(DI/64)*GCH, 256, 0, stream>>>(
-      dtvb, ub, xz_b, xdbl, A_log, Dp, carry, y_b);
-  gemm_outp_k<<<dim3(CM/128, (BLr+63)/64, 2), 256, 0, stream>>>(
-      y_b, out_w_b, x, cat_b);
-  gemm_gate_k<<<dim3(CM/64, (BLr+63)/64, 1), 256, 0, stream>>>(
-      cat_b, gate_w_b, gate_b, mix_b);
-  gemm_proj_k<<<dim3(CM/64, (BLr+63)/64, 1), 256, 0, stream>>>(
-      mix_b, proj_w_b, proj_b, out);
-}
+  hipMemsetAsync(wsb + O_BAR, 0, 64*sizeof(int), stream);
+  mega_k<<<NB, 256, 0, stream>>>(
+      x, norm_w, in_w, conv_w, conv_b, xp_w, dt_w, dt_b, A_log, Dp,
+      out_w, gate_w, gate_b, proj_w, proj_b, out, wsb);
+}
```

Result: slower. 1.039 ms (+226.9%).
